# Performance work log

Hardware: AMD Instinct MI355X
Metric: run time of the kernel (lower is better)

## Reference

```python
import jax, jax.numpy as jnp
import numpy as np
from jax import lax

N_ANCHOR = 9
FEAT_STRIDE = 16
N_PRE_NMS = 2000
N_POST_NMS = 300
NMS_THRESH = 0.7
MIN_SIZE = 16.0
SCALE = 1.0


def generate_anchor(feat_stride, h, w):
    # base anchors: scales {8,16,32} x ratios {0.5,1,2}, (y1,x1,y2,x2)
    base = float(feat_stride)
    ratios = jnp.array([0.5, 1.0, 2.0], jnp.float32)
    scales = jnp.array([8.0, 16.0, 32.0], jnp.float32)
    py = px = base / 2.0
    hs = base * scales[None, :] * jnp.sqrt(ratios)[:, None]          # [3,3]
    ws = base * scales[None, :] * jnp.sqrt(1.0 / ratios)[:, None]    # [3,3]
    anchor_base = jnp.stack([py - hs / 2, px - ws / 2, py + hs / 2, px + ws / 2], axis=-1).reshape(9, 4)
    shift_y = jnp.arange(h, dtype=jnp.float32) * feat_stride
    shift_x = jnp.arange(w, dtype=jnp.float32) * feat_stride
    sy, sx = jnp.meshgrid(shift_y, shift_x, indexing='ij')
    shifts = jnp.stack([sy, sx, sy, sx], axis=-1).reshape(-1, 1, 4)  # [h*w,1,4]
    return (shifts + anchor_base[None]).reshape(-1, 4)               # [h*w*9,4]


def loc2bbox(anchor, loc):
    ah = anchor[:, 2] - anchor[:, 0]
    aw = anchor[:, 3] - anchor[:, 1]
    acy = anchor[:, 0] + 0.5 * ah
    acx = anchor[:, 1] + 0.5 * aw
    dy, dx, dh, dw = loc[:, 0], loc[:, 1], loc[:, 2], loc[:, 3]
    cy = dy * ah + acy
    cx = dx * aw + acx
    h = jnp.exp(dh) * ah
    w = jnp.exp(dw) * aw
    return jnp.stack([cy - 0.5 * h, cx - 0.5 * w, cy + 0.5 * h, cx + 0.5 * w], axis=1)


def nms_keep(boxes, thresh):
    # boxes sorted by descending score; returns keep mask
    y1, x1, y2, x2 = boxes[:, 0], boxes[:, 1], boxes[:, 2], boxes[:, 3]
    area = (y2 - y1) * (x2 - x1)
    yy1 = jnp.maximum(y1[:, None], y1[None, :])
    xx1 = jnp.maximum(x1[:, None], x1[None, :])
    yy2 = jnp.minimum(y2[:, None], y2[None, :])
    xx2 = jnp.minimum(x2[:, None], x2[None, :])
    inter = jnp.clip(yy2 - yy1, 0.0) * jnp.clip(xx2 - xx1, 0.0)
    iou = inter / (area[:, None] + area[None, :] - inter + 1e-9)
    n = boxes.shape[0]

    def step(supp, i):
        keep_i = jnp.logical_not(supp[i])
        supp = supp | (keep_i & (iou[i] > thresh))
        return supp, keep_i

    _, keep = lax.scan(step, jnp.zeros((n,), bool), jnp.arange(n))
    return keep


def proposal_single(loc, score, anchor, img_h, img_w):
    roi = loc2bbox(anchor, loc)
    roi = jnp.stack([
        jnp.clip(roi[:, 0], 0.0, img_h),
        jnp.clip(roi[:, 1], 0.0, img_w),
        jnp.clip(roi[:, 2], 0.0, img_h),
        jnp.clip(roi[:, 3], 0.0, img_w)], axis=1)
    hs = roi[:, 2] - roi[:, 0]
    ws = roi[:, 3] - roi[:, 1]
    ms = MIN_SIZE * SCALE
    score = jnp.where((hs >= ms) & (ws >= ms), score, -jnp.inf)
    top_s, idx = lax.top_k(score, N_PRE_NMS)
    boxes = roi[idx]
    keep = nms_keep(boxes, NMS_THRESH) & jnp.isfinite(top_s)
    order = jnp.argsort(jnp.logical_not(keep), stable=True)[:N_POST_NMS]
    out = boxes[order]
    kout = keep[order]
    return jnp.where(kout[:, None], out, 0.0), kout


def _conv(x, w, b, pad):
    y = lax.conv_general_dilated(x, w, (1, 1), pad, dimension_numbers=('NCHW', 'OIHW', 'NCHW'))
    return y + b[None, :, None, None]


def setup_inputs() -> dict:
    key = jax.random.key(0)
    ks = jax.random.split(key, 7)
    n, c, h, w = 8, 512, 64, 64
    x = jax.random.normal(ks[0], (n, c, h, w), jnp.float32)
    conv_w = 0.01 * jax.random.normal(ks[1], (512, c, 3, 3), jnp.float32)
    conv_b = 0.01 * jax.random.normal(ks[2], (512,), jnp.float32)
    score_w = 0.01 * jax.random.normal(ks[3], (2 * N_ANCHOR, 512, 1, 1), jnp.float32)
    score_b = 0.01 * jax.random.normal(ks[4], (2 * N_ANCHOR,), jnp.float32)
    params_w = 0.01 * jax.random.normal(ks[5], (4 * N_ANCHOR, 512, 1, 1), jnp.float32)
    params_b = 0.01 * jax.random.normal(ks[6], (4 * N_ANCHOR,), jnp.float32)
    return {"x": x, "conv_w": conv_w, "conv_b": conv_b, "score_w": score_w, "score_b": score_b,
            "params_w": params_w, "params_b": params_b, "img_h": 1024, "img_w": 1024}


def reference(x, conv_w, conv_b, score_w, score_b, params_w, params_b, img_h, img_w):
    n, _, h, w = x.shape
    anchor = generate_anchor(FEAT_STRIDE, h, w)                       # [h*w*9,4]
    mid = jax.nn.relu(_conv(x, conv_w, conv_b, 'SAME'))               # [n,512,h,w]
    rpn_params = _conv(mid, params_w, params_b, 'VALID')              # [n,36,h,w]
    rpn_params = rpn_params.transpose(0, 2, 3, 1).reshape(n, -1, 4)   # [n,h*w*9,4]
    rpn_score = _conv(mid, score_w, score_b, 'VALID')                 # [n,18,h,w]
    rpn_score = rpn_score.transpose(0, 2, 3, 1).reshape(n, -1, 2)     # [n,h*w*9,2]
    fg_score = jax.nn.softmax(rpn_score, axis=2)[:, :, 1]             # [n,h*w*9]
    rois, keep = jax.vmap(lambda l, s: proposal_single(l, s, anchor, float(img_h), float(img_w)))(rpn_params, fg_score)
    roi_index = jnp.repeat(jnp.arange(n, dtype=jnp.int32), N_POST_NMS)
    rois = rois.reshape(-1, 4)
    return rpn_params, rpn_score, rois, roi_index, anchor


if __name__ == '__main__':
    out = reference(**setup_inputs())
    print([o.shape for o in out])
```

## Files before the change

### kernel.cpp

```cpp
#include <hip/hip_runtime.h>
#include <math.h>

typedef _Float16 f16x8 __attribute__((ext_vector_type(8)));
typedef float f32x4 __attribute__((ext_vector_type(4)));
typedef unsigned long long u64;

#define OUT_PARAMS 0L
#define OUT_SCORE  1179648L
#define OUT_ROIS   1769472L
#define OUT_IDX    1779072L
#define OUT_ANCH   1781472L

#define WS_WT2   0L
#define WS_W2H   27648L
#define WS_W2L   1207296L
#define WS_XT    2386944L
#define WS_MID   19164160L
#define WS_FG    35941376L
#define WS_KEYS  36236288L
#define WS_BOX   36531200L
#define WS_SELK  37710848L
#define WS_SBOX  37727232L
#define WS_SUPP  37792768L

__global__ void k_transpose_w(const float* __restrict__ conv_w,
                              const float* __restrict__ score_w,
                              const float* __restrict__ params_w,
                              _Float16* __restrict__ W2h, _Float16* __restrict__ W2l,
                              float* __restrict__ wt2) {
  int e = blockIdx.x * 256 + threadIdx.x;
  if (e < 9 * 512 * 512) {
    int tap = e >> 18, rem = e & 262143;
    int oc = rem >> 9, c = rem & 511;
    float v = conv_w[(oc * 512 + c) * 9 + tap] * 1024.0f;
    _Float16 h = (_Float16)v;
    W2h[e] = h;
    W2l[e] = (_Float16)(v - (float)h);
  }
  if (e < 512 * 54) {
    int o = e % 54, c = e / 54;
    wt2[e] = (o < 18) ? score_w[o * 512 + c] : params_w[(o - 18) * 512 + c];
  }
}

__global__ __launch_bounds__(256) void k_split_x(const float* __restrict__ x,
                                                 float* __restrict__ Xt) {
  __shared__ float t[64][66];
  const int pxb = blockIdx.x;
  const int c0  = blockIdx.y * 64;
  const int n   = blockIdx.z;
  const int tid = threadIdx.x;
  const int a = tid >> 6, b = tid & 63;
#pragma unroll
  for (int i = 0; i < 16; ++i) {
    int c_l = i * 4 + a;
    t[c_l][b] = x[((size_t)(n * 512 + c0 + c_l) * 4096) + pxb * 64 + b];
  }
  __syncthreads();
#pragma unroll
  for (int i = 0; i < 16; ++i) {
    int px_l = i * 4 + a;
    Xt[((size_t)(n * 4096 + pxb * 64 + px_l) * 512) + c0 + b] = t[b][px_l];
  }
}

__global__ __launch_bounds__(256, 2) void k_conv_mfma(
    const float* __restrict__ Xt, const _Float16* __restrict__ W2h,
    const _Float16* __restrict__ W2l, const float* __restrict__ bias,
    float* __restrict__ mid) {
  __shared__ _Float16 XH[8448];
  __shared__ _Float16 XL[8448];

  const int n   = blockIdx.x >> 5;
  const int rp  = blockIdx.x & 31;
  const int oc0 = blockIdx.y * 128;
  const int tid = threadIdx.x;
  const int lane = tid & 63, wid = tid >> 6;
  const int wm = wid >> 1, wn = wid & 1;
  const int l15 = lane & 15, kg = lane >> 4;

  f32x4 acch[4][4], accl[4][4];
#pragma unroll
  for (int i = 0; i < 4; ++i)
#pragma unroll
    for (int j = 0; j < 4; ++j) {
      acch[i][j] = (f32x4){0.f, 0.f, 0.f, 0.f};
      accl[i][j] = (f32x4){0.f, 0.f, 0.f, 0.f};
    }

  for (int cb = 0; cb < 16; ++cb) {
    __syncthreads();
    for (int u = tid; u < 1056; u += 256) {
      const int px = u >> 2, sd = u & 3;
      const int cg = sd ^ ((px >> 1) & 3);
      const int hrow = px / 66, hcol = px - hrow * 66;
      const int y = rp * 2 - 1 + hrow, xx = hcol - 1;
      float4 v0 = {0.f, 0.f, 0.f, 0.f}, v1 = {0.f, 0.f, 0.f, 0.f};
      if ((unsigned)y < 64u && (unsigned)xx < 64u) {
        const float* s = Xt + (((size_t)(n * 64 + y) * 64 + xx) * 512 + cb * 32 + cg * 8);
        v0 = *(const float4*)s;
        v1 = *(const float4*)(s + 4);
      }
      f16x8 hv, lv;
      float f[8] = {v0.x, v0.y, v0.z, v0.w, v1.x, v1.y, v1.z, v1.w};
#pragma unroll
      for (int e = 0; e < 8; ++e) {
        const float fs = f[e] * 512.0f;
        _Float16 h = (_Float16)fs;
        hv[e] = h;
        lv[e] = (_Float16)(fs - (float)h);
      }
      *(f16x8*)(XH + u * 8) = hv;
      *(f16x8*)(XL + u * 8) = lv;
    }
    __syncthreads();

#pragma unroll
    for (int ky = 0; ky < 3; ++ky) {
#pragma unroll
      for (int kx = 0; kx < 3; ++kx) {
        const int tap = ky * 3 + kx;
        f16x8 ah[4], al[4], bh[4], bl[4];
#pragma unroll
        for (int mf = 0; mf < 4; ++mf) {
          const size_t aoff =
              ((size_t)(tap * 512 + oc0 + wm * 64 + mf * 16 + l15)) * 512 + cb * 32 + kg * 8;
          ah[mf] = *(const f16x8*)(W2h + aoff);
          al[mf] = *(const f16x8*)(W2l + aoff);
        }
#pragma unroll
        for (int nf = 0; nf < 4; ++nf) {
          const int lpx = (wn + ky) * 66 + nf * 16 + l15 + kx;
          const int off = lpx * 32 + ((kg ^ ((lpx >> 1) & 3)) * 8);
          bh[nf] = *(const f16x8*)(XH + off);
          bl[nf] = *(const f16x8*)(XL + off);
        }
#pragma unroll
        for (int mf = 0; mf < 4; ++mf)
#pragma unroll
          for (int nf = 0; nf < 4; ++nf) {
            acch[mf][nf] = __builtin_amdgcn_mfma_f32_16x16x32_f16(ah[mf], bh[nf], acch[mf][nf], 0, 0, 0);
            accl[mf][nf] = __builtin_amdgcn_mfma_f32_16x16x32_f16(ah[mf], bl[nf], accl[mf][nf], 0, 0, 0);
            accl[mf][nf] = __builtin_amdgcn_mfma_f32_16x16x32_f16(al[mf], bh[nf], accl[mf][nf], 0, 0, 0);
          }
      }
    }
  }

  const float inv = 1.0f / (1024.0f * 512.0f);
  const int y = rp * 2 + wn;
#pragma unroll
  for (int mf = 0; mf < 4; ++mf) {
#pragma unroll
    for (int r = 0; r < 4; ++r) {
      const int oc = oc0 + wm * 64 + mf * 16 + kg * 4 + r;
      const float bv = bias[oc];
      float* mp = mid + (((size_t)(n * 512 + oc) * 64 + y) * 64);
#pragma unroll
      for (int nf = 0; nf < 4; ++nf) {
        const int xcol = nf * 16 + l15;
        mp[xcol] = fmaxf((acch[mf][nf][r] + accl[mf][nf][r]) * inv + bv, 0.f);
      }
    }
  }
}

__global__ __launch_bounds__(256) void k_1x1(
    const float* __restrict__ mid, const float* __restrict__ wt2,
    const float* __restrict__ score_b, const float* __restrict__ params_b,
    float* __restrict__ out, float* __restrict__ fg) {
  const int p = blockIdx.x * 256 + threadIdx.x;
  const int n = p >> 12, hw = p & 4095;
  float acc[54];
#pragma unroll
  for (int o = 0; o < 54; ++o) acc[o] = 0.f;
  const float* m = mid + (size_t)n * 512 * 4096 + hw;
  for (int c = 0; c < 512; ++c) {
    const float mv = m[(size_t)c * 4096];
    const float* w = wt2 + c * 54;
#pragma unroll
    for (int o = 0; o < 54; ++o) acc[o] = fmaf(w[o], mv, acc[o]);
  }
#pragma unroll
  for (int o = 0; o < 18; ++o) acc[o] += score_b[o];
#pragma unroll
  for (int o = 0; o < 36; ++o) acc[18 + o] += params_b[o];

  float* so = out + OUT_SCORE + (size_t)n * 73728 + (size_t)hw * 18;
#pragma unroll
  for (int o = 0; o < 18; ++o) so[o] = acc[o];
  float* po = out + OUT_PARAMS + (size_t)n * 147456 + (size_t)hw * 36;
#pragma unroll
  for (int o = 0; o < 36; ++o) po[o] = acc[18 + o];
  float* f = fg + (size_t)n * 36864 + hw * 9;
#pragma unroll
  for (int a = 0; a < 9; ++a) {
    float d = acc[a * 2 + 1] - acc[a * 2 + 0];
    f[a] = 1.f / (1.f + expf(-d));
  }
}

__global__ void k_proposals(const float* __restrict__ out_params,
                            const float* __restrict__ fg,
                            const int* __restrict__ ih_p, const int* __restrict__ iw_p,
                            float* __restrict__ boxes, unsigned int* __restrict__ keys,
                            float* __restrict__ anchor_out) {
  const int g = blockIdx.x * 256 + threadIdx.x;
  if (g >= 8 * 36864) return;
  const int n = g / 36864, i = g % 36864;
  const int hw = i / 9, a = i % 9;
  const float ih = (float)ih_p[0], iw = (float)iw_p[0];
  const float ratios[3] = {0.5f, 1.f, 2.f};
  const float scales[3] = {8.f, 16.f, 32.f};
  const float rr = ratios[a / 3], sc = scales[a % 3];
  const float hs = (16.f * sc) * sqrtf(rr);
  const float ws_ = (16.f * sc) * sqrtf(1.f / rr);
  const float sy = (float)((hw >> 6) * 16);
  const float sx = (float)((hw & 63) * 16);
  const float ay1 = sy + (8.f - hs * 0.5f), ax1 = sx + (8.f - ws_ * 0.5f);
  const float ay2 = sy + (8.f + hs * 0.5f), ax2 = sx + (8.f + ws_ * 0.5f);
  if (n == 0) {
    float4 av; av.x = ay1; av.y = ax1; av.z = ay2; av.w = ax2;
    *(float4*)&anchor_out[(size_t)i * 4] = av;
  }
  const float ah = ay2 - ay1, aw = ax2 - ax1;
  const float acy = ay1 + 0.5f * ah, acx = ax1 + 0.5f * aw;
  const float* loc = out_params + (size_t)n * 147456 + (size_t)i * 4;
  const float dy = loc[0], dx = loc[1], dh = loc[2], dw = loc[3];
  const float cy = dy * ah + acy, cx = dx * aw + acx;
  const float h = expf(dh) * ah, w = expf(dw) * aw;
  const float y1 = fminf(fmaxf(cy - 0.5f * h, 0.f), ih);
  const float x1 = fminf(fmaxf(cx - 0.5f * w, 0.f), iw);
  const float y2 = fminf(fmaxf(cy + 0.5f * h, 0.f), ih);
  const float x2 = fminf(fmaxf(cx + 0.5f * w, 0.f), iw);
  float4 bx; bx.x = y1; bx.y = x1; bx.z = y2; bx.w = x2;
  *(float4*)&boxes[(size_t)g * 4] = bx;
  float s = fg[g];
  if (!((y2 - y1) >= 16.f && (x2 - x1) >= 16.f)) s = -INFINITY;
  const unsigned int b = __float_as_uint(s);
  keys[g] = (b & 0x80000000u) ? ~b : (b | 0x80000000u);
}

__global__ __launch_bounds__(256) void k_select(
    const unsigned int* __restrict__ keys, const float* __restrict__ boxes,
    unsigned int* __restrict__ selkey, float* __restrict__ sboxes) {
  __shared__ unsigned int hist[4][256];
  __shared__ unsigned long long sel[4096];
  __shared__ unsigned int s_prefix, s_remk, s_cnt;
  const int n = blockIdx.x, tid = threadIdx.x;
  const unsigned int* kk = keys + (size_t)n * 36864;
  if (tid == 0) { s_prefix = 0; s_remk = 2000; s_cnt = 0; }
  const int hslot = tid >> 6;

  for (int byte = 3; byte >= 0; --byte) {
    for (int b2 = tid; b2 < 1024; b2 += 256) ((unsigned int*)hist)[b2] = 0;
    __syncthreads();
    const unsigned pfx = s_prefix;
    const unsigned hmask = (byte == 3) ? 0u : (0xFFFFFFFFu << ((byte + 1) * 8));
    for (int i2 = tid; i2 < 36864; i2 += 256) {
      const unsigned k = kk[i2];
      if ((k & hmask) == (pfx & hmask))
        atomicAdd(&hist[hslot][(k >> (byte * 8)) & 255], 1u);
    }
    __syncthreads();
    if (tid == 0) {
      unsigned rem = s_remk;
      int b2 = 255;
      for (;; --b2) {
        const unsigned c2 = hist[0][b2] + hist[1][b2] + hist[2][b2] + hist[3][b2];
        if (c2 >= rem) break;
        rem -= c2;
      }
      s_prefix = pfx | ((unsigned)b2 << (byte * 8));
      s_remk = rem;
    }
    __syncthreads();
  }
  const unsigned T = s_prefix;

  for (int i2 = tid; i2 < 36864; i2 += 256) {
    const unsigned k = kk[i2];
    if (k >= T) {
      const unsigned p2 = atomicAdd(&s_cnt, 1u);
      if (p2 < 4096)
        sel[p2] = ((unsigned long long)k << 32) | (unsigned)(~i2);
    }
  }
  __syncthreads();
  unsigned cnt = s_cnt; if (cnt > 4096) cnt = 4096;
  for (int i2 = (int)cnt + tid; i2 < 4096; i2 += 256) sel[i2] = 0ull;

  for (int k2 = 2; k2 <= 4096; k2 <<= 1) {
    for (int j = k2 >> 1; j > 0; j >>= 1) {
      __syncthreads();
      for (int t = tid; t < 2048; t += 256) {
        const int i1 = (t << 1) - (t & (j - 1));
        const int i2 = i1 + j;
        const unsigned long long va = sel[i1], vb = sel[i2];
        const bool sw = ((i1 & k2) == 0) ? (va < vb) : (va > vb);
        if (sw) { sel[i1] = vb; sel[i2] = va; }
      }
    }
  }
  __syncthreads();

  for (int s2 = tid; s2 < 2048; s2 += 256) {
    const unsigned long long comp = sel[s2];
    unsigned key = (unsigned)(comp >> 32);
    unsigned idx = ~(unsigned)(comp & 0xFFFFFFFFu);
    float4 bx; bx.x = 0.f; bx.y = 0.f; bx.z = 0.f; bx.w = 0.f;
    if (comp != 0ull) bx = *(const float4*)&boxes[((size_t)n * 36864 + idx) * 4];
    else key = 0;
    selkey[n * 2048 + s2] = key;
    *(float4*)&sboxes[((size_t)n * 2048 + s2) * 4] = bx;
  }
}

__global__ void k_nms_matrix(const float* __restrict__ sboxes,
                             unsigned long long* __restrict__ supp) {
  const int t = blockIdx.x * 256 + threadIdx.x;
  if (t >= 8 * 2000 * 32) return;
  const int n = t / 64000, rem = t % 64000;
  const int i = rem >> 5, w = rem & 31;
  const float4 bi = *(const float4*)&sboxes[((size_t)n * 2048 + i) * 4];
  const float areai = (bi.z - bi.x) * (bi.w - bi.y);
  unsigned long long bits = 0ull;
  const int j0 = w * 64;
  for (int jj = 0; jj < 64; ++jj) {
    const int j = j0 + jj;
    if (j >= 2000) break;
    const float4 bj = *(const float4*)&sboxes[((size_t)n * 2048 + j) * 4];
    const float areaj = (bj.z - bj.x) * (bj.w - bj.y);
    const float yy1 = fmaxf(bi.x, bj.x), xx1 = fmaxf(bi.y, bj.y);
    const float yy2 = fminf(bi.z, bj.z), xx2 = fminf(bi.w, bj.w);
    const float ih2 = fmaxf(yy2 - yy1, 0.f), iw2 = fmaxf(xx2 - xx1, 0.f);
    const float inter = ih2 * iw2;
    const float iou = inter / (areai + areaj - inter + 1e-9f);
    if (iou > 0.7f) bits |= (1ull << jj);
  }
  supp[((size_t)n * 2000 + i) * 32 + w] = bits;
}

__global__ void k_nms_scan(const unsigned long long* __restrict__ supp,
                           const unsigned int* __restrict__ selkey,
                           const float* __restrict__ sboxes,
                           float* __restrict__ out) {
  const int n = blockIdx.x;
  const int lane = threadIdx.x;
  const unsigned long long* sp = supp + (size_t)n * 64000;
  const bool ld = lane < 32;
  unsigned long long removed = 0ull, keepmask = 0ull;
#define LDROW(i) (ld ? sp[(size_t)(i) * 32 + lane] : 0ull)
  unsigned long long r0 = LDROW(0), r1 = LDROW(1), r2 = LDROW(2), r3 = LDROW(3),
                     r4 = LDROW(4), r5 = LDROW(5), r6 = LDROW(6), r7 = LDROW(7);
  for (int g = 0; g < 250; ++g) {
    unsigned long long n0 = 0, n1 = 0, n2 = 0, n3 = 0, n4 = 0, n5 = 0, n6 = 0, n7 = 0;
    if (g < 249) {
      const int nb = (g + 1) * 8;
      n0 = LDROW(nb); n1 = LDROW(nb + 1); n2 = LDROW(nb + 2); n3 = LDROW(nb + 3);
      n4 = LDROW(nb + 4); n5 = LDROW(nb + 5); n6 = LDROW(nb + 6); n7 = LDROW(nb + 7);
    }
#define STEP(K, RK)                                                       \
    {                                                                     \
      const int i = g * 8 + K;                                            \
      const unsigned long long remw = __shfl(removed, i >> 6);            \
      if (!((remw >> (i & 63)) & 1ull)) {                                 \
        if (ld) removed |= RK;                                            \
        if (lane == (i >> 6)) keepmask |= (1ull << (i & 63));             \
      }                                                                   \
    }
    STEP(0, r0) STEP(1, r1) STEP(2, r2) STEP(3, r3)
    STEP(4, r4) STEP(5, r5) STEP(6, r6) STEP(7, r7)
#undef STEP
    r0 = n0; r1 = n1; r2 = n2; r3 = n3; r4 = n4; r5 = n5; r6 = n6; r7 = n7;
  }
#undef LDROW
  int running = 0;
  for (int ci = 0; ci < 32; ++ci) {
    const unsigned long long km = __shfl(keepmask, ci);
    const int i = ci * 64 + lane;
    const unsigned key = selkey[n * 2048 + i];
    const bool fin = (key >= 0x80000000u);
    const bool kf = (((km >> lane) & 1ull) != 0ull) && fin;
    const unsigned long long ball = __ballot(kf);
    const int rank = running + __popcll(ball & ((1ull << lane) - 1ull));
    if (kf && rank < 300) {
      const float4 bx = *(const float4*)&sboxes[((size_t)n * 2048 + i) * 4];
      *(float4*)&out[OUT_ROIS + ((size_t)n * 300 + rank) * 4] = bx;
    }
    running += __popcll(ball);
  }
  const int kept = running < 300 ? running : 300;
  for (int r2 = kept + lane; r2 < 300; r2 += 64) {
    float4 z; z.x = 0.f; z.y = 0.f; z.z = 0.f; z.w = 0.f;
    *(float4*)&out[OUT_ROIS + ((size_t)n * 300 + r2) * 4] = z;
  }
  for (int r2 = lane; r2 < 300; r2 += 64)
    out[OUT_IDX + n * 300 + r2] = (float)n;
}

extern "C" void kernel_launch(void* const* d_in, const int* in_sizes, int n_in,
                              void* d_out, int out_size, void* d_ws, size_t ws_size,
                              hipStream_t stream) {
  const float* x        = (const float*)d_in[0];
  const float* conv_w   = (const float*)d_in[1];
  const float* conv_b   = (const float*)d_in[2];
  const float* score_w  = (const float*)d_in[3];
  const float* score_b  = (const float*)d_in[4];
  const float* params_w = (const float*)d_in[5];
  const float* params_b = (const float*)d_in[6];
  const int*   ih       = (const int*)d_in[7];
  const int*   iw       = (const int*)d_in[8];
  float* out = (float*)d_out;
  float* ws  = (float*)d_ws;

  float* wt2 = ws + WS_WT2;
  _Float16* W2h = (_Float16*)(ws + WS_W2H);
  _Float16* W2l = (_Float16*)(ws + WS_W2L);
  float* Xt  = ws + WS_XT;
  float* mid = ws + WS_MID;
  float* fg  = ws + WS_FG;
  unsigned int* keys = (unsigned int*)(ws + WS_KEYS);
  float* boxes = ws + WS_BOX;
  unsigned int* selkey = (unsigned int*)(ws + WS_SELK);
  float* sboxes = ws + WS_SBOX;
  u64* supp = (u64*)(ws + WS_SUPP);

  hipLaunchKernelGGL(k_transpose_w, dim3(9216), dim3(256), 0, stream,
                     conv_w, score_w, params_w, W2h, W2l, wt2);
  hipLaunchKernelGGL(k_split_x, dim3(64, 8, 8), dim3(256), 0, stream, x, Xt);
  hipLaunchKernelGGL(k_conv_mfma, dim3(256, 4), dim3(256), 0, stream,
                     Xt, W2h, W2l, conv_b, mid);
  hipLaunchKernelGGL(k_1x1, dim3(128), dim3(256), 0, stream,
                     mid, wt2, score_b, params_b, out, fg);
  hipLaunchKernelGGL(k_proposals, dim3(1152), dim3(256), 0, stream,
                     out + OUT_PARAMS, fg, ih, iw, boxes, keys, out + OUT_ANCH);
  hipLaunchKernelGGL(k_select, dim3(8), dim3(256), 0, stream,
                     keys, boxes, selkey, sboxes);
  hipLaunchKernelGGL(k_nms_matrix, dim3(2000), dim3(256), 0, stream,
                     sboxes, supp);
  hipLaunchKernelGGL(k_nms_scan, dim3(8), dim3(64), 0, stream,
                     supp, selkey, sboxes, out);
}
```

Before: 1.487 ms.

## Prefetch next conv input chunk into registers; widen and warp-aggregate k_select

The conv kernel now loads the next channel block of the input into registers while MFMAs run on the current shared-memory tile, so global load latency overlaps compute instead of being exposed before every block. Separately, k_select goes from 256 to 1024 threads per block, uses 16 histogram slots, and aggregates histogram and compaction atomics per wavefront with ballots. The prefetch raises register pressure (ten extra float4 registers), which may lower occupancy in the conv kernel. The ballot-based peer matching adds instructions per element in exchange for fewer contended atomics.

```diff
diff --git a/kernel.cpp b/kernel.cpp
--- a/kernel.cpp
+++ b/kernel.cpp
@@ -88,32 +88,56 @@
       accl[i][j] = (f32x4){0.f, 0.f, 0.f, 0.f};
     }
 
+  float4 stA[5], stB[5];
+
+#define LOADX(CB)                                                              \
+  {                                                                            \
+    _Pragma("unroll") for (int k = 0; k < 5; ++k) {                            \
+      const int u = tid + k * 256;                                             \
+      float4 a4 = {0.f, 0.f, 0.f, 0.f}, b4 = {0.f, 0.f, 0.f, 0.f};            \
+      if (k < 4 || u < 1056) {                                                 \
+        const int px = u >> 2, sd = u & 3;                                     \
+        const int cg = sd ^ ((px >> 1) & 3);                                   \
+        const int hrow = px / 66, hcol = px - hrow * 66;                       \
+        const int y = rp * 2 - 1 + hrow, xx = hcol - 1;                        \
+        if ((unsigned)y < 64u && (unsigned)xx < 64u) {                         \
+          const float* s =                                                     \
+              Xt + (((size_t)(n * 64 + y) * 64 + xx) * 512 + (CB) * 32 + cg * 8); \
+          a4 = *(const float4*)s;                                              \
+          b4 = *(const float4*)(s + 4);                                        \
+        }                                                                      \
+      }                                                                        \
+      stA[k] = a4; stB[k] = b4;                                                \
+    }                                                                          \
+  }
+
+#define STOREX()                                                               \
+  {                                                                            \
+    _Pragma("unroll") for (int k = 0; k < 5; ++k) {                            \
+      const int u = tid + k * 256;                                             \
+      if (k < 4 || u < 1056) {                                                 \
+        float f[8] = {stA[k].x, stA[k].y, stA[k].z, stA[k].w,                  \
+                      stB[k].x, stB[k].y, stB[k].z, stB[k].w};                 \
+        f16x8 hv, lv;                                                          \
+        _Pragma("unroll") for (int e = 0; e < 8; ++e) {                        \
+          const float fs = f[e] * 512.0f;                                      \
+          const _Float16 h = (_Float16)fs;                                     \
+          hv[e] = h;                                                           \
+          lv[e] = (_Float16)(fs - (float)h);                                   \
+        }                                                                      \
+        *(f16x8*)(XH + u * 8) = hv;                                            \
+        *(f16x8*)(XL + u * 8) = lv;                                            \
+      }                                                                        \
+    }                                                                          \
+  }
+
+  LOADX(0);
+
   for (int cb = 0; cb < 16; ++cb) {
     __syncthreads();
-    for (int u = tid; u < 1056; u += 256) {
-      const int px = u >> 2, sd = u & 3;
-      const int cg = sd ^ ((px >> 1) & 3);
-      const int hrow = px / 66, hcol = px - hrow * 66;
-      const int y = rp * 2 - 1 + hrow, xx = hcol - 1;
-      float4 v0 = {0.f, 0.f, 0.f, 0.f}, v1 = {0.f, 0.f, 0.f, 0.f};
-      if ((unsigned)y < 64u && (unsigned)xx < 64u) {
-        const float* s = Xt + (((size_t)(n * 64 + y) * 64 + xx) * 512 + cb * 32 + cg * 8);
-        v0 = *(const float4*)s;
-        v1 = *(const float4*)(s + 4);
-      }
-      f16x8 hv, lv;
-      float f[8] = {v0.x, v0.y, v0.z, v0.w, v1.x, v1.y, v1.z, v1.w};
-#pragma unroll
-      for (int e = 0; e < 8; ++e) {
-        const float fs = f[e] * 512.0f;
-        _Float16 h = (_Float16)fs;
-        hv[e] = h;
-        lv[e] = (_Float16)(fs - (float)h);
-      }
-      *(f16x8*)(XH + u * 8) = hv;
-      *(f16x8*)(XL + u * 8) = lv;
-    }
-    __syncthreads();
+    STOREX();
+    __syncthreads();
+    if (cb < 15) LOADX(cb + 1);
 
 #pragma unroll
     for (int ky = 0; ky < 3; ++ky) {
@@ -132,8 +156,8 @@
         for (int nf = 0; nf < 4; ++nf) {
           const int lpx = (wn + ky) * 66 + nf * 16 + l15 + kx;
           const int off = lpx * 32 + ((kg ^ ((lpx >> 1) & 3)) * 8);
-          bh[nf] = *(const f16x8*)(XH + off);
-          bl[nf] = *(const f16x8*)(XL + off);
+          bh[nf] = *(const f16x8*)(&XH[off]);
+          bl[nf] = *(const f16x8*)(&XL[off]);
         }
 #pragma unroll
         for (int mf = 0; mf < 4; ++mf)
@@ -146,6 +170,8 @@
       }
     }
   }
+#undef LOADX
+#undef STOREX
 
   const float inv = 1.0f / (1024.0f * 512.0f);
   const int y = rp * 2 + wn;
@@ -241,33 +267,51 @@
   keys[g] = (b & 0x80000000u) ? ~b : (b | 0x80000000u);
 }
 
-__global__ __launch_bounds__(256) void k_select(
+__global__ __launch_bounds__(1024) void k_select(
     const unsigned int* __restrict__ keys, const float* __restrict__ boxes,
     unsigned int* __restrict__ selkey, float* __restrict__ sboxes) {
-  __shared__ unsigned int hist[4][256];
+  __shared__ unsigned int hist[16][256];
   __shared__ unsigned long long sel[4096];
   __shared__ unsigned int s_prefix, s_remk, s_cnt;
   const int n = blockIdx.x, tid = threadIdx.x;
+  const int lane = tid & 63;
   const unsigned int* kk = keys + (size_t)n * 36864;
   if (tid == 0) { s_prefix = 0; s_remk = 2000; s_cnt = 0; }
   const int hslot = tid >> 6;
 
   for (int byte = 3; byte >= 0; --byte) {
-    for (int b2 = tid; b2 < 1024; b2 += 256) ((unsigned int*)hist)[b2] = 0;
+    for (int b2 = tid; b2 < 4096; b2 += 1024) ((unsigned int*)hist)[b2] = 0;
     __syncthreads();
     const unsigned pfx = s_prefix;
     const unsigned hmask = (byte == 3) ? 0u : (0xFFFFFFFFu << ((byte + 1) * 8));
-    for (int i2 = tid; i2 < 36864; i2 += 256) {
+    for (int i2 = tid; i2 < 36864; i2 += 1024) {
       const unsigned k = kk[i2];
-      if ((k & hmask) == (pfx & hmask))
-        atomicAdd(&hist[hslot][(k >> (byte * 8)) & 255], 1u);
+      if ((k & hmask) == (pfx & hmask)) {
+        const unsigned b8 = (k >> (byte * 8)) & 255u;
+        unsigned long long peers = __ballot(1);
+#pragma unroll
+        for (int bit = 0; bit < 8; ++bit) {
+          const unsigned long long bb = __ballot((b8 >> bit) & 1u);
+          peers &= ((b8 >> bit) & 1u) ? bb : ~bb;
+        }
+        peers &= __ballot(1);
+        if (lane == __builtin_ctzll(peers))
+          atomicAdd(&hist[hslot][b8], (unsigned)__popcll(peers));
+      }
+    }
+    __syncthreads();
+    if (tid < 256) {
+      unsigned s2 = 0;
+#pragma unroll
+      for (int j = 0; j < 16; ++j) s2 += hist[j][tid];
+      hist[0][tid] = s2;
     }
     __syncthreads();
     if (tid == 0) {
       unsigned rem = s_remk;
       int b2 = 255;
       for (;; --b2) {
-        const unsigned c2 = hist[0][b2] + hist[1][b2] + hist[2][b2] + hist[3][b2];
+        const unsigned c2 = hist[0][b2];
         if (c2 >= rem) break;
         rem -= c2;
       }
@@ -278,22 +322,27 @@
   }
   const unsigned T = s_prefix;
 
-  for (int i2 = tid; i2 < 36864; i2 += 256) {
+  for (int i2 = tid; i2 < 36864; i2 += 1024) {
     const unsigned k = kk[i2];
     if (k >= T) {
-      const unsigned p2 = atomicAdd(&s_cnt, 1u);
+      const unsigned long long m = __ballot(1);
+      const int ldr = __builtin_ctzll(m);
+      unsigned basep = 0;
+      if (lane == ldr) basep = atomicAdd(&s_cnt, (unsigned)__popcll(m));
+      basep = __shfl(basep, ldr);
+      const unsigned p2 = basep + (unsigned)__popcll(m & ((1ull << lane) - 1ull));
       if (p2 < 4096)
         sel[p2] = ((unsigned long long)k << 32) | (unsigned)(~i2);
     }
   }
   __syncthreads();
   unsigned cnt = s_cnt; if (cnt > 4096) cnt = 4096;
-  for (int i2 = (int)cnt + tid; i2 < 4096; i2 += 256) sel[i2] = 0ull;
+  for (int i2 = (int)cnt + tid; i2 < 4096; i2 += 1024) sel[i2] = 0ull;
 
   for (int k2 = 2; k2 <= 4096; k2 <<= 1) {
     for (int j = k2 >> 1; j > 0; j >>= 1) {
       __syncthreads();
-      for (int t = tid; t < 2048; t += 256) {
+      for (int t = tid; t < 2048; t += 1024) {
         const int i1 = (t << 1) - (t & (j - 1));
         const int i2 = i1 + j;
         const unsigned long long va = sel[i1], vb = sel[i2];
@@ -304,7 +353,7 @@
   }
   __syncthreads();
 
-  for (int s2 = tid; s2 < 2048; s2 += 256) {
+  for (int s2 = tid; s2 < 2048; s2 += 1024) {
     const unsigned long long comp = sel[s2];
     unsigned key = (unsigned)(comp >> 32);
     unsigned idx = ~(unsigned)(comp & 0xFFFFFFFFu);
@@ -435,7 +484,7 @@
                      mid, wt2, score_b, params_b, out, fg);
   hipLaunchKernelGGL(k_proposals, dim3(1152), dim3(256), 0, stream,
                      out + OUT_PARAMS, fg, ih, iw, boxes, keys, out + OUT_ANCH);
-  hipLaunchKernelGGL(k_select, dim3(8), dim3(256), 0, stream,
+  hipLaunchKernelGGL(k_select, dim3(8), dim3(1024), 0, stream,
                      keys, boxes, selkey, sboxes);
   hipLaunchKernelGGL(k_nms_matrix, dim3(2000), dim3(256), 0, stream,
                      sboxes, supp);
```

New measurement: 1.568 ms. 1.05x slower.
